# Kernel tuning notes

Measured on AMD Instinct MI355X. Metric: run time of the kernel, lower is better.

The kernel has to match this reference:

```python
import jax, jax.numpy as jnp
import numpy as np

CUTOFF = 5.0
N_GAUSS = 32
N_HEADS = 8
MAX_Z = 100


def _gather(feat, idx):
    # feat: (B, N, ...), idx: (B, N, K) -> (B, N, K, ...)
    return jax.vmap(lambda f, i: f[i])(feat, idx)


def setup_inputs() -> dict:
    key = jax.random.key(0)
    ks = jax.random.split(key, 10)
    B, N, K, D, G = 16, 512, 48, 128, N_GAUSS
    s = 0.05
    positions = jax.random.normal(ks[0], (B, N, 3), dtype=jnp.float32) * 2.0
    z = jax.random.randint(ks[1], (B, N), 0, MAX_Z)
    neighbors = jax.random.randint(ks[2], (B, N, K), 0, N)
    neighbor_mask = jnp.ones((B, N, K), dtype=jnp.float32)
    embedding = jax.random.normal(ks[3], (MAX_Z, D), jnp.float32)
    embedding = embedding.at[0].set(0.0)  # padding_idx=0
    filt_W = jax.random.normal(ks[4], (G, D), jnp.float32) * s
    filt_b = jnp.zeros((D,), jnp.float32)
    Wq = jax.random.normal(ks[5], (D, D), jnp.float32) * s
    Wk = jax.random.normal(ks[6], (D, D), jnp.float32) * s
    Wv = jax.random.normal(ks[7], (D, D), jnp.float32) * s
    Wo = jax.random.normal(ks[8], (D, D), jnp.float32) * s
    return dict(positions=positions, z=z, neighbors=neighbors,
                neighbor_mask=neighbor_mask, embedding=embedding,
                filt_W=filt_W, filt_b=filt_b, Wq=Wq, Wk=Wk, Wv=Wv, Wo=Wo)


def reference(positions, z, neighbors, neighbor_mask, embedding,
              filt_W, filt_b, Wq, Wk, Wv, Wo):
    B, N, K = neighbors.shape
    D = embedding.shape[1]
    H = N_HEADS
    hd = D // H

    # atom embeddings
    x = embedding[z]                                        # (B, N, D)

    # AtomDistances: neighbor gather + distances
    pos_j = _gather(positions, neighbors)                   # (B, N, K, 3)
    r_vec = pos_j - positions[:, :, None, :]
    r_ij = jnp.sqrt(jnp.sum(r_vec * r_vec, axis=-1) + 1e-12)  # (B, N, K)

    # Positional_Embedding: prepend self-distance 0.01, log-normal smearing
    r_iij = jnp.concatenate(
        [jnp.full((B, N, 1), 0.01, r_ij.dtype), r_ij], axis=-1)  # (B, N, K+1)
    offsets = jnp.linspace(np.log(0.1), np.log(CUTOFF), N_GAUSS).astype(r_ij.dtype)
    width = offsets[1] - offsets[0]
    coeff = -0.5 / (width * width)
    f_iij = jnp.exp(coeff * (jnp.log(r_iij)[..., None] - offsets) ** 2)  # (B,N,K+1,G)

    # filter network + cosine cutoff
    W = f_iij @ filt_W + filt_b                             # (B, N, K+1, D)
    C = 0.5 * (jnp.cos(r_iij * jnp.pi / CUTOFF) + 1.0) * (r_iij < CUTOFF)
    W = W * C[..., None]

    # gather neighbor embeddings, include self (ego) node
    x_j = _gather(x, neighbors)                             # (B, N, K, D)
    nodes = jnp.concatenate([x[:, :, None, :], x_j], axis=2)  # (B, N, K+1, D)
    kv_in = nodes * W

    # EgoAttention: center atom attends over {self + neighbors}
    q = (x @ Wq).reshape(B, N, H, hd)
    k = (kv_in @ Wk).reshape(B, N, K + 1, H, hd)
    v = (kv_in @ Wv).reshape(B, N, K + 1, H, hd)
    scores = jnp.einsum('bnhd,bnkhd->bnhk', q, k) / jnp.sqrt(jnp.float32(hd))
    mask = jnp.concatenate(
        [jnp.ones((B, N, 1), neighbor_mask.dtype), neighbor_mask], axis=-1)
    scores = jnp.where(mask[:, :, None, :] > 0, scores, jnp.float32(-1e9))
    attn = jax.nn.softmax(scores, axis=-1)
    agg = jnp.einsum('bnhk,bnkhd->bnhd', attn, v).reshape(B, N, D)
    v_msg = agg @ Wo

    # residual update (apply_transition_function=False): x = x + v
    return x + v_msg
```

## Files before the change

### kernel.cpp

```cpp
#include <hip/hip_runtime.h>
#include <math.h>

#define NTHREADS 256

typedef _Float16 v8h __attribute__((ext_vector_type(8)));
typedef float    v4f __attribute__((ext_vector_type(4)));

namespace {
constexpr int D   = 128;
constexpr int H   = 8;
constexpr int KNB = 48;
constexpr int KP1 = 49;
constexpr int NN  = 512;

constexpr size_t WS_P    = 0;
constexpr size_t WS_QKZ  = 16777216;
constexpr size_t WS_WVOT = 16982016;
constexpr size_t WS_QZ   = 17244160;
constexpr size_t WS_FWTP = 17295360;
constexpr size_t WS_EMBH = 17303552;
constexpr size_t WS_NEED = 17329152;

constexpr float LOG_LO = -2.302585092994046f;
constexpr float LOG_HI =  1.609437912434100f;
constexpr float GWIDTH = (LOG_HI - LOG_LO) / 31.0f;
constexpr float GCOEFF = -0.5f / (GWIDTH * GWIDTH);
constexpr float PI_OVER_CUT = 3.14159265358979323846f / 5.0f;
}

union H8U4 { _Float16 h[8]; uint4 u; };
union H4U2 { _Float16 h[4]; uint2 u; };

__global__ __launch_bounds__(NTHREADS) void k0a_qz(
    const float* __restrict__ embedding, const float* __restrict__ Wq,
    float* __restrict__ qz) {
  const int idx = blockIdx.x * NTHREADS + threadIdx.x;
  const int zz = idx >> 7, j = idx & 127;
  float a0 = 0.f, a1 = 0.f, a2 = 0.f, a3 = 0.f;
  for (int e = 0; e < 128; e += 4) {
    a0 = fmaf(embedding[zz * 128 + e + 0], Wq[(e + 0) * 128 + j], a0);
    a1 = fmaf(embedding[zz * 128 + e + 1], Wq[(e + 1) * 128 + j], a1);
    a2 = fmaf(embedding[zz * 128 + e + 2], Wq[(e + 2) * 128 + j], a2);
    a3 = fmaf(embedding[zz * 128 + e + 3], Wq[(e + 3) * 128 + j], a3);
  }
  qz[idx] = (a0 + a1) + (a2 + a3);
}

__global__ __launch_bounds__(NTHREADS) void k0b_prep(
    const float* __restrict__ filt_W, const float* __restrict__ Wk,
    const float* __restrict__ Wv, const float* __restrict__ Wo,
    const float* __restrict__ qz, const float* __restrict__ embedding,
    _Float16* __restrict__ QKz, _Float16* __restrict__ WvoT,
    _Float16* __restrict__ fWTP, _Float16* __restrict__ embh) {
  const int blk = blockIdx.x;
  const int tid = threadIdx.x;
  if (blk < 400) {
    const int idx = blk * NTHREADS + tid;
    const int zz = idx >> 10, hc = idx & 1023, h = hc >> 7, c = hc & 127;
    float acc = 0.0f;
#pragma unroll
    for (int e = 0; e < 16; ++e)
      acc = fmaf(qz[zz * 128 + h * 16 + e], Wk[c * 128 + h * 16 + e], acc);
    QKz[idx] = (_Float16)(acc * 0.25f);
  } else if (blk < 912) {
    const int idx = (blk - 400) * NTHREADS + tid;
    const int cp = idx >> 10, kk = idx & 1023, d = kk >> 3, h = kk & 7;
    float acc = 0.0f;
#pragma unroll
    for (int cc = 0; cc < 16; ++cc)
      acc = fmaf(Wv[d * 128 + h * 16 + cc], Wo[(h * 16 + cc) * 128 + cp], acc);
    WvoT[idx] = (_Float16)acc;
  } else if (blk < 914) {
    const int i = (blk - 912) * NTHREADS + tid;
    const int nt = i >> 6, quad = (i >> 4) & 3, col = i & 15;
    H8U4 pk;
#pragma unroll
    for (int j = 0; j < 8; ++j)
      pk.h[j] = (_Float16)filt_W[(quad * 8 + j) * 128 + nt * 16 + col];
    *(uint4*)&fWTP[i * 8] = pk.u;
  } else {
    const int idx = (blk - 914) * NTHREADS + tid;
    embh[idx] = (_Float16)embedding[idx];
  }
}

namespace k2c {
constexpr int KVT_S = 72;
constexpr int QK_S  = 136;
constexpr int ATH_S = 72;
constexpr int SC_S  = 52;
constexpr int OFF_KVT = 0;
constexpr int OFF_QK  = 18432;
constexpr int OFF_ATH = 20608;
constexpr int OFF_SC  = 21904;
constexpr int OFF_LR  = 23568;
constexpr int OFF_C   = 23776;
constexpr int OFF_MSK = 23984;
constexpr int OFF_ZJ  = 24192;
constexpr int SMEM    = 24400;
}

__global__ __launch_bounds__(NTHREADS, 6) void k2_attn(
    const float* __restrict__ positions, const int* __restrict__ z,
    const int* __restrict__ neighbors, const float* __restrict__ nmask,
    const _Float16* __restrict__ embh, const float* __restrict__ filt_b,
    const _Float16* __restrict__ fWTP, const _Float16* __restrict__ QKz,
    _Float16* __restrict__ P) {
  using namespace k2c;
  __shared__ __align__(16) char smem[SMEM];
  _Float16* s_kvT = reinterpret_cast<_Float16*>(smem + OFF_KVT);
  _Float16* s_qk  = reinterpret_cast<_Float16*>(smem + OFF_QK);
  _Float16* s_ath = reinterpret_cast<_Float16*>(smem + OFF_ATH);
  float*    s_sc  = reinterpret_cast<float*>(smem + OFF_SC);
  float*    s_lr  = reinterpret_cast<float*>(smem + OFF_LR);
  float*    s_C   = reinterpret_cast<float*>(smem + OFF_C);
  float*    s_msk = reinterpret_cast<float*>(smem + OFF_MSK);
  int*      s_zj  = reinterpret_cast<int*>(smem + OFF_ZJ);

  const int a   = blockIdx.x;
  const int b   = a >> 9;
  const int n   = a & (NN - 1);
  const int tid = threadIdx.x;
  const int w    = tid >> 6;
  const int lane = tid & 63;
  const int col  = lane & 15;
  const int quad = lane >> 4;

  const int zc = __builtin_amdgcn_readfirstlane(z[a]);

  if (tid < KP1) {
    int j; float m;
    if (tid == 0) { j = n; m = 1.0f; }
    else { j = neighbors[a * KNB + tid - 1]; m = nmask[a * KNB + tid - 1]; }
    float r;
    if (tid == 0) r = 0.01f;
    else {
      const float dx = positions[(b * NN + j) * 3 + 0] - positions[a * 3 + 0];
      const float dy = positions[(b * NN + j) * 3 + 1] - positions[a * 3 + 1];
      const float dz = positions[(b * NN + j) * 3 + 2] - positions[a * 3 + 2];
      r = sqrtf(dx * dx + dy * dy + dz * dz + 1e-12f);
    }
    s_lr[tid]  = __logf(r);
    s_C[tid]   = (r < 5.0f) ? (0.5f * (__cosf(r * PI_OVER_CUT) + 1.0f)) : 0.0f;
    s_msk[tid] = m;
    s_zj[tid]  = z[b * NN + j];
  } else if (tid >= 128) {
    const int i = tid - 128;
    const uint4 v = *(const uint4*)(QKz + (size_t)zc * 1024 + i * 8);
    const int h = i >> 4, dd = (i & 15) * 8;
    *(uint4*)&s_qk[h * QK_S + dd] = v;
  }
  __syncthreads();

  {
    const int trow = 16 * w + col;
    const float lr = s_lr[trow < KP1 ? trow : KP1 - 1];
    v8h afrag;
#pragma unroll
    for (int j = 0; j < 8; ++j) {
      const int g = quad * 8 + j;
      const float dlt = lr - (LOG_LO + (float)g * GWIDTH);
      afrag[j] = (_Float16)__expf(GCOEFF * dlt * dlt);
    }
    v4f acc[8];
#pragma unroll
    for (int nt = 0; nt < 8; ++nt) {
      const v8h bfrag = *(const v8h*)(fWTP + (((nt * 4 + quad) * 16 + col) * 8));
      v4f zero = {0.0f, 0.0f, 0.0f, 0.0f};
      acc[nt] = __builtin_amdgcn_mfma_f32_16x16x32_f16(afrag, bfrag, zero, 0, 0, 0);
    }
    float bv[8];
#pragma unroll
    for (int nt = 0; nt < 8; ++nt) bv[nt] = filt_b[nt * 16 + col];
    const int t0 = 16 * w + quad * 4;
    float cf4[4]; int zj4[4];
#pragma unroll
    for (int reg = 0; reg < 4; ++reg) {
      const int t = t0 + reg;
      const bool valid = t < KP1;
      cf4[reg] = valid ? s_C[t] : 0.0f;
      zj4[reg] = s_zj[valid ? t : KP1 - 1];
    }
    const int slot_log = 2 * w + (quad >> 1);
    const int elem     = (quad & 1) * 4;
#pragma unroll
    for (int nt = 0; nt < 8; ++nt) {
      const int c = nt * 16 + col;
      const int phys = slot_log ^ ((c >> 3) & 7);
      H4U2 pk;
#pragma unroll
      for (int reg = 0; reg < 4; ++reg) {
        const float ev = (float)embh[(size_t)zj4[reg] * D + c];
        pk.h[reg] = (_Float16)((acc[nt][reg] + bv[nt]) * cf4[reg] * ev);
      }
      *(uint2*)&s_kvT[c * KVT_S + phys * 8 + elem] = pk.u;
    }
  }
  __syncthreads();

  {
    v4f sacc = {0.0f, 0.0f, 0.0f, 0.0f};
    const int slot_log = 2 * w + (col >> 3);
    const int elem     = col & 7;
#pragma unroll
    for (int ks = 0; ks < 4; ++ks) {
      v8h afr;
#pragma unroll
      for (int j = 0; j < 8; ++j) {
        const int c = ks * 32 + quad * 8 + j;
        const int phys = slot_log ^ ((c >> 3) & 7);
        afr[j] = s_kvT[c * KVT_S + phys * 8 + elem];
      }
      const v8h bfr = *(const v8h*)&s_qk[col * QK_S + ks * 32 + quad * 8];
      sacc = __builtin_amdgcn_mfma_f32_16x16x32_f16(afr, bfr, sacc, 0, 0, 0);
    }
    const int h = col;
    if (h < H) {
#pragma unroll
      for (int reg = 0; reg < 4; ++reg) {
        const int t = 16 * w + quad * 4 + reg;
        if (t < KP1) {
          float sc = sacc[reg];
          if (s_msk[t] <= 0.0f) sc = -1e9f;
          s_sc[h * SC_S + t] = sc;
        }
      }
    }
  }
  __syncthreads();

  if (tid < 64) {
    const int h  = tid >> 3;
    const int sl = tid & 7;
    float* row = &s_sc[h * SC_S];
    float m = -1e30f;
    for (int t = sl; t < KP1; t += 8) m = fmaxf(m, row[t]);
    m = fmaxf(m, __shfl_xor(m, 1));
    m = fmaxf(m, __shfl_xor(m, 2));
    m = fmaxf(m, __shfl_xor(m, 4));
    float s = 0.0f;
    float ev[7];
#pragma unroll
    for (int i = 0; i < 7; ++i) {
      const int t = sl + i * 8;
      const float e = (t < KP1) ? __expf(row[t] - m) : 0.0f;
      ev[i] = e;
      s += e;
    }
    s += __shfl_xor(s, 1);
    s += __shfl_xor(s, 2);
    s += __shfl_xor(s, 4);
    const float inv = 1.0f / s;
#pragma unroll
    for (int i = 0; i < 7; ++i) {
      const int t = sl + i * 8;
      if (t < KP1) s_ath[h * ATH_S + t] = (_Float16)(ev[i] * inv);
    }
  } else if (tid < 128) {
    const int i = tid - 64;
    for (int idx = i; idx < 8 * 15; idx += 64) {
      const int h = idx / 15;
      const int t = KP1 + idx % 15;
      s_ath[h * ATH_S + t] = (_Float16)0.0f;
    }
  }
  __syncthreads();

  {
    const int arow = (col < 8) ? col : 8;
    const v8h a0 = *(const v8h*)&s_ath[arow * ATH_S + quad * 8];
    const v8h a1 = *(const v8h*)&s_ath[arow * ATH_S + 32 + quad * 8];
#pragma unroll
    for (int nti = 0; nti < 2; ++nti) {
      const int c = (2 * w + nti) * 16 + col;
      const int xr = (c >> 3) & 7;
      const v8h b0 = *(const v8h*)&s_kvT[c * KVT_S + ((quad)     ^ xr) * 8];
      const v8h b1 = *(const v8h*)&s_kvT[c * KVT_S + ((4 + quad) ^ xr) * 8];
      v4f pacc = {0.0f, 0.0f, 0.0f, 0.0f};
      pacc = __builtin_amdgcn_mfma_f32_16x16x32_f16(a0, b0, pacc, 0, 0, 0);
      pacc = __builtin_amdgcn_mfma_f32_16x16x32_f16(a1, b1, pacc, 0, 0, 0);
      if (quad < 2) {
        H4U2 pk;
#pragma unroll
        for (int reg = 0; reg < 4; ++reg) pk.h[reg] = (_Float16)pacc[reg];
        *(uint2*)(P + (size_t)a * 1024 + c * 8 + quad * 4) = pk.u;
      }
    }
  }
}

__global__ __launch_bounds__(NTHREADS) void k3_gemm(
    const int* __restrict__ z, const float* __restrict__ embedding,
    const _Float16* __restrict__ P, const _Float16* __restrict__ WvoT,
    float* __restrict__ out) {
  __shared__ __align__(16) _Float16 sA[16 * 136];
  __shared__ __align__(16) _Float16 sB[64 * 136];
  __shared__ int s_z[16];
  const int a0 = (blockIdx.x >> 1) * 16;
  const int n0 = (blockIdx.x & 1) * 64;
  const int tid = threadIdx.x;
  const int w    = tid >> 6;
  const int lane = tid & 63;
  const int col  = lane & 15;
  const int quad = lane >> 4;
  if (tid < 16) s_z[tid] = z[a0 + tid];

  v4f acc = (v4f){0.f, 0.f, 0.f, 0.f};

  for (int kc = 0; kc < 8; ++kc) {
    const int k0 = kc * 128;
    __syncthreads();
    {
      const int ai = tid >> 4, sl = tid & 15;
      *(uint4*)&sA[ai * 136 + sl * 8] =
          *(const uint4*)(P + (size_t)(a0 + ai) * 1024 + k0 + sl * 8);
    }
#pragma unroll
    for (int it = 0; it < 4; ++it) {
      const int idx = it * NTHREADS + tid;
      const int cp = idx >> 4, sl = idx & 15;
      *(uint4*)&sB[cp * 136 + sl * 8] =
          *(const uint4*)(WvoT + (size_t)(n0 + cp) * 1024 + k0 + sl * 8);
    }
    __syncthreads();
#pragma unroll
    for (int ks = 0; ks < 4; ++ks) {
      const v8h af = *(const v8h*)&sA[col * 136 + ks * 32 + quad * 8];
      const v8h bf = *(const v8h*)&sB[(w * 16 + col) * 136 + ks * 32 + quad * 8];
      acc = __builtin_amdgcn_mfma_f32_16x16x32_f16(af, bf, acc, 0, 0, 0);
    }
  }
#pragma unroll
  for (int reg = 0; reg < 4; ++reg) {
    const int al = quad * 4 + reg;
    const int cp = n0 + w * 16 + col;
    out[(size_t)(a0 + al) * 128 + cp] =
        embedding[(size_t)s_z[al] * 128 + cp] + acc[reg];
  }
}

namespace mono {
constexpr int KV_S = 136, QK_S = 136, FWT_S = 40, ATH_S = 64, SC_S = 52, P_S = 132;
constexpr int OFF_KV = 0, OFF_FWT = 17408, OFF_P = 17408, OFF_AGG = 21632,
              OFF_QK = 27648, OFF_ATH = 32000, OFF_SC = 34048, OFF_Q = 35712,
              OFF_LR = 36224, OFF_C = 36432, OFF_MSK = 36640, OFF_ZJ = 36848,
              SMEM = 37056;
}

__global__ __launch_bounds__(NTHREADS, 4) void tdt_mono(
    const float* __restrict__ positions, const int* __restrict__ z,
    const int* __restrict__ neighbors, const float* __restrict__ nmask,
    const float* __restrict__ embedding, const float* __restrict__ filt_W,
    const float* __restrict__ filt_b, const float* __restrict__ Wq,
    const float* __restrict__ Wk, const float* __restrict__ Wv,
    const float* __restrict__ Wo, float* __restrict__ out) {
  using namespace mono;
  __shared__ __align__(16) char smem[SMEM];
  _Float16* s_kvh = reinterpret_cast<_Float16*>(smem + OFF_KV);
  _Float16* s_fWT = reinterpret_cast<_Float16*>(smem + OFF_FWT);
  float*    s_p   = reinterpret_cast<float*>(smem + OFF_P);
  float*    s_agg = reinterpret_cast<float*>(smem + OFF_AGG);
  _Float16* s_qkh = reinterpret_cast<_Float16*>(smem + OFF_QK);
  _Float16* s_ath = reinterpret_cast<_Float16*>(smem + OFF_ATH);
  float*    s_sc  = reinterpret_cast<float*>(smem + OFF_SC);
  float*    s_q   = reinterpret_cast<float*>(smem + OFF_Q);
  float*    s_lr  = reinterpret_cast<float*>(smem + OFF_LR);
  float*    s_C   = reinterpret_cast<float*>(smem + OFF_C);
  float*    s_msk = reinterpret_cast<float*>(smem + OFF_MSK);
  int*      s_zj  = reinterpret_cast<int*>(smem + OFF_ZJ);
  const int a = blockIdx.x, b = a >> 9, n = a & (NN - 1), tid = threadIdx.x;
  const int w = tid >> 6, lane = tid & 63, col = lane & 15, quad = lane >> 4;
  const int zc = __builtin_amdgcn_readfirstlane(z[a]);
  if (tid < KP1) {
    int j; float m;
    if (tid == 0) { j = n; m = 1.0f; }
    else { j = neighbors[a * KNB + tid - 1]; m = nmask[a * KNB + tid - 1]; }
    float r;
    if (tid == 0) r = 0.01f;
    else {
      const float dx = positions[(b * NN + j) * 3 + 0] - positions[a * 3 + 0];
      const float dy = positions[(b * NN + j) * 3 + 1] - positions[a * 3 + 1];
      const float dz = positions[(b * NN + j) * 3 + 2] - positions[a * 3 + 2];
      r = sqrtf(dx * dx + dy * dy + dz * dz + 1e-12f);
    }
    s_lr[tid] = __logf(r);
    s_C[tid] = (r < 5.0f) ? (0.5f * (__cosf(r * PI_OVER_CUT) + 1.0f)) : 0.0f;
    s_msk[tid] = m;
    s_zj[tid] = z[b * NN + j];
  } else if (tid >= 64 && tid < 128) {
    const int i = tid - 64;
    for (int rep = 0; rep < 64; ++rep) {
      const int idx = rep * 64 + i;
      const int g = idx >> 7, c = idx & 127;
      s_fWT[c * FWT_S + g] = (_Float16)filt_W[idx];
    }
    unsigned* kz = reinterpret_cast<unsigned*>(s_kvh);
    for (int d0 = KP1 * (KV_S / 2) + i; d0 < 64 * (KV_S / 2); d0 += 64) kz[d0] = 0u;
  } else if (tid >= 128) {
    const int d = tid - 128;
    float acc = 0.0f;
    for (int e = 0; e < D; e += 4) {
      const float x0 = embedding[zc * D + e + 0];
      const float x1 = embedding[zc * D + e + 1];
      const float x2 = embedding[zc * D + e + 2];
      const float x3 = embedding[zc * D + e + 3];
      acc = fmaf(x0, Wq[(e + 0) * D + d], acc);
      acc = fmaf(x1, Wq[(e + 1) * D + d], acc);
      acc = fmaf(x2, Wq[(e + 2) * D + d], acc);
      acc = fmaf(x3, Wq[(e + 3) * D + d], acc);
    }
    s_q[d] = acc;
  }
  __syncthreads();
  {
    const int trow = 16 * w + col;
    const float lr = s_lr[trow < KP1 ? trow : KP1 - 1];
    v8h afrag;
#pragma unroll
    for (int j = 0; j < 8; ++j) {
      const int g = quad * 8 + j;
      const float dlt = lr - (LOG_LO + (float)g * GWIDTH);
      afrag[j] = (_Float16)__expf(GCOEFF * dlt * dlt);
    }
    v4f acc[8];
#pragma unroll
    for (int nt = 0; nt < 8; ++nt) {
      const v8h bfrag = *(const v8h*)&s_fWT[(nt * 16 + col) * FWT_S + quad * 8];
      v4f zero = {0.0f, 0.0f, 0.0f, 0.0f};
      acc[nt] = __builtin_amdgcn_mfma_f32_16x16x32_f16(afrag, bfrag, zero, 0, 0, 0);
    }
    float bv[8];
#pragma unroll
    for (int nt = 0; nt < 8; ++nt) bv[nt] = filt_b[nt * 16 + col];
#pragma unroll
    for (int reg = 0; reg < 4; ++reg) {
      const int t = 16 * w + quad * 4 + reg;
      const bool valid = t < KP1;
      float cf = 0.0f; int zj = 0;
      if (valid) { cf = s_C[t]; zj = s_zj[t]; }
      const float* erow = embedding + (size_t)zj * D;
#pragma unroll
      for (int nt = 0; nt < 8; ++nt) {
        const int c = nt * 16 + col;
        if (valid)
          s_kvh[t * KV_S + c] = (_Float16)((acc[nt][reg] + bv[nt]) * cf * erow[c]);
      }
    }
  }
  {
    const int h = tid & 7;
    const float4 q0 = *(const float4*)&s_q[h * 16 + 0];
    const float4 q1 = *(const float4*)&s_q[h * 16 + 4];
    const float4 q2 = *(const float4*)&s_q[h * 16 + 8];
    const float4 q3 = *(const float4*)&s_q[h * 16 + 12];
#pragma unroll
    for (int it = 0; it < 4; ++it) {
      const int d = ((it * NTHREADS + tid) >> 3);
      const float* wk = &Wk[d * D + h * 16];
      const float4 w0 = *(const float4*)&wk[0];
      const float4 w1 = *(const float4*)&wk[4];
      const float4 w2 = *(const float4*)&wk[8];
      const float4 w3 = *(const float4*)&wk[12];
      float s = w0.x * q0.x;
      s = fmaf(w0.y, q0.y, s); s = fmaf(w0.z, q0.z, s); s = fmaf(w0.w, q0.w, s);
      s = fmaf(w1.x, q1.x, s); s = fmaf(w1.y, q1.y, s);
      s = fmaf(w1.z, q1.z, s); s = fmaf(w1.w, q1.w, s);
      s = fmaf(w2.x, q2.x, s); s = fmaf(w2.y, q2.y, s);
      s = fmaf(w2.z, q2.z, s); s = fmaf(w2.w, q2.w, s);
      s = fmaf(w3.x, q3.x, s); s = fmaf(w3.y, q3.y, s);
      s = fmaf(w3.z, q3.z, s); s = fmaf(w3.w, q3.w, s);
      s_qkh[h * QK_S + d] = (_Float16)s;
    }
  }
  __syncthreads();
  {
    v4f sacc = {0.0f, 0.0f, 0.0f, 0.0f};
#pragma unroll
    for (int ks = 0; ks < 4; ++ks) {
      const v8h afr = *(const v8h*)&s_kvh[(16 * w + col) * KV_S + ks * 32 + quad * 8];
      const v8h bfr = *(const v8h*)&s_qkh[col * QK_S + ks * 32 + quad * 8];
      sacc = __builtin_amdgcn_mfma_f32_16x16x32_f16(afr, bfr, sacc, 0, 0, 0);
    }
    const int h = col;
    if (h < H) {
#pragma unroll
      for (int reg = 0; reg < 4; ++reg) {
        const int t = 16 * w + quad * 4 + reg;
        if (t < KP1) {
          float sc = sacc[reg] * 0.25f;
          if (s_msk[t] <= 0.0f) sc = -1e9f;
          s_sc[h * SC_S + t] = sc;
        }
      }
    }
  }
  __syncthreads();
  if (tid < 64) {
    const int h = tid >> 3, sl = tid & 7;
    float* row = &s_sc[h * SC_S];
    float m = -1e30f;
    for (int t = sl; t < KP1; t += 8) m = fmaxf(m, row[t]);
    m = fmaxf(m, __shfl_xor(m, 1));
    m = fmaxf(m, __shfl_xor(m, 2));
    m = fmaxf(m, __shfl_xor(m, 4));
    float s = 0.0f;
    float ev[7];
#pragma unroll
    for (int i = 0; i < 7; ++i) {
      const int t = sl + i * 8;
      const float e = (t < KP1) ? __expf(row[t] - m) : 0.0f;
      ev[i] = e; s += e;
    }
    s += __shfl_xor(s, 1);
    s += __shfl_xor(s, 2);
    s += __shfl_xor(s, 4);
    const float inv = 1.0f / s;
#pragma unroll
    for (int i = 0; i < 7; ++i) {
      const int t = sl + i * 8;
      if (t < KP1) s_ath[h * ATH_S + t] = (_Float16)(ev[i] * inv);
    }
  } else if (tid < 128) {
    const int i = tid - 64;
    for (int idx = i; idx < 8 * 15; idx += 64) {
      const int h = idx / 15, t = KP1 + idx % 15;
      s_ath[h * ATH_S + t] = (_Float16)0.0f;
    }
  }
  __syncthreads();
  {
    const v8h a0 = *(const v8h*)&s_ath[col * ATH_S + quad * 8];
    const v8h a1 = *(const v8h*)&s_ath[col * ATH_S + 32 + quad * 8];
#pragma unroll
    for (int nti = 0; nti < 2; ++nti) {
      const int c = (2 * w + nti) * 16 + col;
      v8h b0, b1;
#pragma unroll
      for (int j = 0; j < 8; ++j) {
        b0[j] = s_kvh[(quad * 8 + j) * KV_S + c];
        b1[j] = s_kvh[(32 + quad * 8 + j) * KV_S + c];
      }
      v4f pacc = {0.0f, 0.0f, 0.0f, 0.0f};
      pacc = __builtin_amdgcn_mfma_f32_16x16x32_f16(a0, b0, pacc, 0, 0, 0);
      pacc = __builtin_amdgcn_mfma_f32_16x16x32_f16(a1, b1, pacc, 0, 0, 0);
#pragma unroll
      for (int reg = 0; reg < 4; ++reg) {
        const int h = quad * 4 + reg;
        if (h < H) s_p[h * P_S + c] = pacc[reg];
      }
    }
  }
  __syncthreads();
  if (tid < 128) {
    const int c = tid;
    const float* pr = &s_p[(c >> 4) * P_S];
    float acc = 0.0f;
    for (int d = 0; d < D; d += 4) {
      const float4 p4 = *(const float4*)&pr[d];
      acc = fmaf(p4.x, Wv[(d + 0) * D + c], acc);
      acc = fmaf(p4.y, Wv[(d + 1) * D + c], acc);
      acc = fmaf(p4.z, Wv[(d + 2) * D + c], acc);
      acc = fmaf(p4.w, Wv[(d + 3) * D + c], acc);
    }
    s_agg[c] = acc;
  }
  __syncthreads();
  if (tid < 128) {
    const int c = tid;
    float acc = embedding[zc * D + c];
    for (int e = 0; e < D; e += 4) {
      const float4 g4 = *(const float4*)&s_agg[e];
      acc = fmaf(g4.x, Wo[(e + 0) * D + c], acc);
      acc = fmaf(g4.y, Wo[(e + 1) * D + c], acc);
      acc = fmaf(g4.z, Wo[(e + 2) * D + c], acc);
      acc = fmaf(g4.w, Wo[(e + 3) * D + c], acc);
    }
    out[a * D + c] = acc;
  }
}

extern "C" void kernel_launch(void* const* d_in, const int* in_sizes, int n_in,
                              void* d_out, int out_size, void* d_ws, size_t ws_size,
                              hipStream_t stream) {
  const float* positions = (const float*)d_in[0];
  const int*   z         = (const int*)d_in[1];
  const int*   neighbors = (const int*)d_in[2];
  const float* nmask     = (const float*)d_in[3];
  const float* embedding = (const float*)d_in[4];
  const float* filt_W    = (const float*)d_in[5];
  const float* filt_b    = (const float*)d_in[6];
  const float* Wq        = (const float*)d_in[7];
  const float* Wk        = (const float*)d_in[8];
  const float* Wv        = (const float*)d_in[9];
  const float* Wo        = (const float*)d_in[10];
  float* out = (float*)d_out;
  const int natoms = in_sizes[1];

  if (ws_size >= WS_NEED) {
    char* ws = (char*)d_ws;
    _Float16* P    = (_Float16*)(ws + WS_P);
    _Float16* QKz  = (_Float16*)(ws + WS_QKZ);
    _Float16* WvoT = (_Float16*)(ws + WS_WVOT);
    float*    qz   = (float*)(ws + WS_QZ);
    _Float16* fWTP = (_Float16*)(ws + WS_FWTP);
    _Float16* embh = (_Float16*)(ws + WS_EMBH);
    k0a_qz<<<50, NTHREADS, 0, stream>>>(embedding, Wq, qz);
    k0b_prep<<<964, NTHREADS, 0, stream>>>(filt_W, Wk, Wv, Wo, qz, embedding,
                                           QKz, WvoT, fWTP, embh);
    k2_attn<<<natoms, NTHREADS, 0, stream>>>(positions, z, neighbors, nmask,
                                             embh, filt_b, fWTP, QKz, P);
    k3_gemm<<<natoms / 16 * 2, NTHREADS, 0, stream>>>(z, embedding, P, WvoT, out);
  } else {
    tdt_mono<<<natoms, NTHREADS, 0, stream>>>(positions, z, neighbors, nmask,
                                              embedding, filt_W, filt_b,
                                              Wq, Wk, Wv, Wo, out);
  }
}
```

Measured before the change: 132.3 us.

## Shrink attention LDS footprint with fp16 scores and aliased buffers, raise occupancy

Scores are stored in shared memory as fp16 instead of fp32, and the attention-weight buffer now aliases the q/k buffer region, which cuts the per-block LDS size. Launch bounds move from 6 to 7 blocks per CU so more blocks can be resident. The kv epilogue is rewritten to use packed half2 arithmetic with the bias folded into the cutoff factor. The trade-off is lower precision in the scores and in the kv products, plus a masked-score sentinel clamped to -60000 to fit the fp16 range. Aliasing is only safe if q/k is no longer read once the attention weights are written.

```diff
diff --git a/kernel.cpp b/kernel.cpp
--- a/kernel.cpp
+++ b/kernel.cpp
@@ -4,6 +4,7 @@
 #define NTHREADS 256
 
 typedef _Float16 v8h __attribute__((ext_vector_type(8)));
+typedef _Float16 h2v __attribute__((ext_vector_type(2)));
 typedef float    v4f __attribute__((ext_vector_type(4)));
 
 namespace {
@@ -91,16 +92,16 @@
 constexpr int SC_S  = 52;
 constexpr int OFF_KVT = 0;
 constexpr int OFF_QK  = 18432;
-constexpr int OFF_ATH = 20608;
-constexpr int OFF_SC  = 21904;
-constexpr int OFF_LR  = 23568;
-constexpr int OFF_C   = 23776;
-constexpr int OFF_MSK = 23984;
-constexpr int OFF_ZJ  = 24192;
-constexpr int SMEM    = 24400;
-}
-
-__global__ __launch_bounds__(NTHREADS, 6) void k2_attn(
+constexpr int OFF_ATH = OFF_QK;
+constexpr int OFF_SC  = 20608;
+constexpr int OFF_LR  = 21440;
+constexpr int OFF_C   = 21648;
+constexpr int OFF_MSK = 21856;
+constexpr int OFF_ZJ  = 22064;
+constexpr int SMEM    = 22272;
+}
+
+__global__ __launch_bounds__(NTHREADS, 7) void k2_attn(
     const float* __restrict__ positions, const int* __restrict__ z,
     const int* __restrict__ neighbors, const float* __restrict__ nmask,
     const _Float16* __restrict__ embh, const float* __restrict__ filt_b,
@@ -111,7 +112,7 @@
   _Float16* s_kvT = reinterpret_cast<_Float16*>(smem + OFF_KVT);
   _Float16* s_qk  = reinterpret_cast<_Float16*>(smem + OFF_QK);
   _Float16* s_ath = reinterpret_cast<_Float16*>(smem + OFF_ATH);
-  float*    s_sc  = reinterpret_cast<float*>(smem + OFF_SC);
+  _Float16* s_sc  = reinterpret_cast<_Float16*>(smem + OFF_SC);
   float*    s_lr  = reinterpret_cast<float*>(smem + OFF_LR);
   float*    s_C   = reinterpret_cast<float*>(smem + OFF_C);
   float*    s_msk = reinterpret_cast<float*>(smem + OFF_MSK);
@@ -181,19 +182,29 @@
       cf4[reg] = valid ? s_C[t] : 0.0f;
       zj4[reg] = s_zj[valid ? t : KP1 - 1];
     }
+    const h2v cf01 = {(_Float16)cf4[0], (_Float16)cf4[1]};
+    const h2v cf23 = {(_Float16)cf4[2], (_Float16)cf4[3]};
     const int slot_log = 2 * w + (quad >> 1);
     const int elem     = (quad & 1) * 4;
 #pragma unroll
     for (int nt = 0; nt < 8; ++nt) {
       const int c = nt * 16 + col;
+      const _Float16 bvh = (_Float16)bv[nt];
+      const h2v cfbv01 = cf01 * bvh;
+      const h2v cfbv23 = cf23 * bvh;
+      const h2v a01 = {(_Float16)acc[nt][0], (_Float16)acc[nt][1]};
+      const h2v a23 = {(_Float16)acc[nt][2], (_Float16)acc[nt][3]};
+      const h2v ev01 = {embh[(size_t)zj4[0] * D + c],
+                        embh[(size_t)zj4[1] * D + c]};
+      const h2v ev23 = {embh[(size_t)zj4[2] * D + c],
+                        embh[(size_t)zj4[3] * D + c]};
+      const h2v kv01 = (a01 * cf01 + cfbv01) * ev01;
+      const h2v kv23 = (a23 * cf23 + cfbv23) * ev23;
+      uint2 u;
+      __builtin_memcpy(&u.x, &kv01, 4);
+      __builtin_memcpy(&u.y, &kv23, 4);
       const int phys = slot_log ^ ((c >> 3) & 7);
-      H4U2 pk;
-#pragma unroll
-      for (int reg = 0; reg < 4; ++reg) {
-        const float ev = (float)embh[(size_t)zj4[reg] * D + c];
-        pk.h[reg] = (_Float16)((acc[nt][reg] + bv[nt]) * cf4[reg] * ev);
-      }
-      *(uint2*)&s_kvT[c * KVT_S + phys * 8 + elem] = pk.u;
+      *(uint2*)&s_kvT[c * KVT_S + phys * 8 + elem] = u;
     }
   }
   __syncthreads();
@@ -220,9 +231,8 @@
       for (int reg = 0; reg < 4; ++reg) {
         const int t = 16 * w + quad * 4 + reg;
         if (t < KP1) {
-          float sc = sacc[reg];
-          if (s_msk[t] <= 0.0f) sc = -1e9f;
-          s_sc[h * SC_S + t] = sc;
+          s_sc[h * SC_S + t] = (s_msk[t] > 0.0f) ? (_Float16)sacc[reg]
+                                                 : (_Float16)(-60000.0f);
         }
       }
     }
@@ -232,9 +242,9 @@
   if (tid < 64) {
     const int h  = tid >> 3;
     const int sl = tid & 7;
-    float* row = &s_sc[h * SC_S];
+    const _Float16* row = &s_sc[h * SC_S];
     float m = -1e30f;
-    for (int t = sl; t < KP1; t += 8) m = fmaxf(m, row[t]);
+    for (int t = sl; t < KP1; t += 8) m = fmaxf(m, (float)row[t]);
     m = fmaxf(m, __shfl_xor(m, 1));
     m = fmaxf(m, __shfl_xor(m, 2));
     m = fmaxf(m, __shfl_xor(m, 4));
@@ -243,7 +253,7 @@
 #pragma unroll
     for (int i = 0; i < 7; ++i) {
       const int t = sl + i * 8;
-      const float e = (t < KP1) ? __expf(row[t] - m) : 0.0f;
+      const float e = (t < KP1) ? __expf((float)row[t] - m) : 0.0f;
       ev[i] = e;
       s += e;
     }
```

After: 130.3 us. No clear change (-1.6%).
